# Kernel tuning notes

Measured on AMD Instinct MI355X. Metric: run time of the kernel, lower is better.

The kernel has to match this reference:

```python
import jax, jax.numpy as jnp
import numpy as np

EPS = 1e-06
NUM_HEADS = 16
HEAD_DIM = 72
HIDDEN = 1152
N = 4096


def _rms_norm(x, weight=None):
    # x: [..., head_dim]; computed in fp32 as in the torch reference
    xf = x.astype(jnp.float32)
    ms = jnp.mean(xf * xf, axis=-1, keepdims=True) + EPS
    y = xf * jax.lax.rsqrt(ms)
    if weight is not None:
        y = y * weight.astype(jnp.float32)
    return y.astype(x.dtype)


def _rotate_half(x):
    h = x.shape[-1] // 2
    return jnp.concatenate([-x[..., h:], x[..., :h]], axis=-1)


def _apply_2d_rope(x, cos, sin):
    # x: [n, H, head_dim]; cos/sin: [n, head_dim] (first half dim-0 freqs, second half dim-1)
    hd = x.shape[-1]
    x1, x2 = x[..., : hd // 2], x[..., hd // 2 :]
    c1, c2 = jnp.split(cos, 2, axis=-1)
    s1, s2 = jnp.split(sin, 2, axis=-1)

    def ap(xp, c, s):
        c = c[:, None, :]  # broadcast over heads (unsqueeze_dim=1)
        s = s[:, None, :]
        return xp * c + _rotate_half(xp) * s

    return jnp.concatenate([ap(x1, c1, s1), ap(x2, c2, s2)], axis=-1)


def setup_inputs() -> dict:
    key = jax.random.key(0)
    ks = jax.random.split(key, 8)
    hidden_states = jax.random.normal(ks[0], (N, HIDDEN), dtype=jnp.float32)
    cos = jax.random.uniform(ks[1], (N, HEAD_DIM), dtype=jnp.float32, minval=-1.0, maxval=1.0)
    sin = jax.random.uniform(ks[2], (N, HEAD_DIM), dtype=jnp.float32, minval=-1.0, maxval=1.0)
    proj = NUM_HEADS * HEAD_DIM
    Wq = jax.random.normal(ks[3], (HIDDEN, proj), dtype=jnp.float32) * 0.02
    Wk = jax.random.normal(ks[4], (HIDDEN, proj), dtype=jnp.float32) * 0.02
    Wv = jax.random.normal(ks[5], (HIDDEN, proj), dtype=jnp.float32) * 0.02
    Wo = jax.random.normal(ks[6], (proj, HIDDEN), dtype=jnp.float32) * 0.02
    q_scale = jnp.ones((HEAD_DIM,), dtype=jnp.float32)
    k_scale = jnp.ones((HEAD_DIM,), dtype=jnp.float32)
    return {
        "hidden_states": hidden_states, "cos": cos, "sin": sin,
        "Wq": Wq, "Wk": Wk, "Wv": Wv, "Wo": Wo,
        "q_scale": q_scale, "k_scale": k_scale,
    }


def reference(hidden_states, cos, sin, Wq, Wk, Wv, Wo, q_scale, k_scale):
    n = hidden_states.shape[0]
    xq = (hidden_states @ Wq).reshape(n, NUM_HEADS, HEAD_DIM)
    xk = (hidden_states @ Wk).reshape(n, NUM_HEADS, HEAD_DIM)
    xv = (hidden_states @ Wv).reshape(n, NUM_HEADS, HEAD_DIM)
    xq = _rms_norm(xq, q_scale)
    xk = _rms_norm(xk, k_scale)
    xv = _rms_norm(xv)  # no scale
    xq = _apply_2d_rope(xq, cos, sin)
    xk = _apply_2d_rope(xk, cos, sin)
    # eager bidirectional attention, scale = 1.0
    attn = jnp.einsum("nhd,mhd->hnm", xq, xk)  # [H, n, n]
    attn = jax.nn.softmax(attn.astype(jnp.float32), axis=-1).astype(xq.dtype)
    out = jnp.einsum("hnm,mhd->nhd", attn, xv)  # [n, H, d]
    out = out.reshape(n, NUM_HEADS * HEAD_DIM)
    return out @ Wo
```

## Files before the change

kernel.cpp:

```cpp
#include <hip/hip_runtime.h>
#include <stdint.h>

typedef unsigned short u16;
typedef __bf16 bf16x8 __attribute__((ext_vector_type(8)));
typedef float f32x4 __attribute__((ext_vector_type(4)));
typedef __attribute__((address_space(1))) const unsigned int as1_u32;
typedef __attribute__((address_space(3))) unsigned int as3_u32;

#define SEQ 4096
#define HID 1152
#define NH 16
#define HD 72

__device__ __forceinline__ void gload_lds16(const void* g, void* l) {
  __builtin_amdgcn_global_load_lds((as1_u32*)g, (as3_u32*)l, 16, 0, 0);
}
__device__ __forceinline__ u16 f2bf(float f) {
  __bf16 h = (__bf16)f;
  return __builtin_bit_cast(u16, h);
}
__device__ __forceinline__ float bf2f(u16 u) {
  unsigned int x = ((unsigned int)u) << 16;
  return __builtin_bit_cast(float, x);
}

__global__ void cvt_x(const float* __restrict__ X, u16* __restrict__ Xb, int n4) {
  int i = blockIdx.x * blockDim.x + threadIdx.x;
  if (i < n4) {
    float4 v = *(const float4*)(X + (size_t)i * 4);
    unsigned int lo = f2bf(v.x) | ((unsigned int)f2bf(v.y) << 16);
    unsigned int hi = f2bf(v.z) | ((unsigned int)f2bf(v.w) << 16);
    *(uint2*)(Xb + (size_t)i * 4) = make_uint2(lo, hi);
  }
}

__global__ void transpose_w(const float* __restrict__ Wq, const float* __restrict__ Wk,
                            const float* __restrict__ Wv, const float* __restrict__ Wo,
                            u16* __restrict__ Wt, u16* __restrict__ Wot) {
  __shared__ __align__(16) float t[32][33];
  int z = blockIdx.z;
  const float* src = (z == 0) ? Wq : (z == 1) ? Wk : (z == 2) ? Wv : Wo;
  u16* dst = (z < 3) ? (Wt + (size_t)z * HID * HID) : Wot;
  int tx = threadIdx.x & 31, ty = threadIdx.x >> 5;
  int c0 = blockIdx.x * 32, r0 = blockIdx.y * 32;
#pragma unroll
  for (int i = 0; i < 4; i++)
    t[ty + i * 8][tx] = src[(size_t)(r0 + ty + i * 8) * HID + c0 + tx];
  __syncthreads();
#pragma unroll
  for (int i = 0; i < 4; i++)
    dst[(size_t)(c0 + ty + i * 8) * HID + r0 + tx] = f2bf(t[tx][ty + i * 8]);
}

template <int OUTBF16>
__global__ __launch_bounds__(256, 2) void gemm_bt(const u16* __restrict__ A,
                                                  const u16* __restrict__ Bt,
                                                  void* __restrict__ Cout,
                                                  int M, int N, int K) {
  __shared__ __align__(16) u16 lds[2][2][128 * 64];
  const int tid = threadIdx.x;
  const int wave = tid >> 6, lane = tid & 63;
  const int l15 = lane & 15, l4 = lane >> 4;
  const size_t bm = (size_t)blockIdx.x * 128, bn = (size_t)blockIdx.y * 128;
  const int wm = (wave >> 1) * 64, wn = (wave & 1) * 64;
  const int nt = K >> 6;

  f32x4 acc[4][4] = {};

  auto stage = [&](int buf, int kt) {
    const int k0 = kt << 6;
#pragma unroll
    for (int r = 0; r < 4; r++) {
      int idx = (r << 8) + tid;
      int m = idx >> 3, j = idx & 7;
      int js = j ^ (m & 7);
      void* ldsA = (void*)&lds[buf][0][(size_t)((r << 8) + (wave << 6)) * 8];
      void* ldsB = (void*)&lds[buf][1][(size_t)((r << 8) + (wave << 6)) * 8];
      gload_lds16(A + (bm + m) * (size_t)K + k0 + js * 8, ldsA);
      gload_lds16(Bt + (bn + m) * (size_t)K + k0 + js * 8, ldsB);
    }
  };

  stage(0, 0);
  for (int t = 0; t < nt; t++) {
    __syncthreads();
    if (t + 1 < nt) stage((t + 1) & 1, t + 1);
    const u16* As = &lds[t & 1][0][0];
    const u16* Bs = &lds[t & 1][1][0];
#pragma unroll
    for (int kk = 0; kk < 2; kk++) {
      bf16x8 af[4], bfr[4];
      int slot = (kk << 2) + l4;
#pragma unroll
      for (int mi = 0; mi < 4; mi++) {
        int m = wm + (mi << 4) + l15;
        af[mi] = *(const bf16x8*)&As[m * 64 + ((slot ^ (m & 7)) << 3)];
      }
#pragma unroll
      for (int ni = 0; ni < 4; ni++) {
        int n = wn + (ni << 4) + l15;
        bfr[ni] = *(const bf16x8*)&Bs[n * 64 + ((slot ^ (n & 7)) << 3)];
      }
#pragma unroll
      for (int mi = 0; mi < 4; mi++)
#pragma unroll
        for (int ni = 0; ni < 4; ni++)
          acc[mi][ni] = __builtin_amdgcn_mfma_f32_16x16x32_bf16(af[mi], bfr[ni], acc[mi][ni], 0, 0, 0);
    }
  }

#pragma unroll
  for (int mi = 0; mi < 4; mi++)
#pragma unroll
    for (int ni = 0; ni < 4; ni++)
#pragma unroll
      for (int r = 0; r < 4; r++) {
        size_t m = bm + wm + (mi << 4) + (l4 << 2) + r;
        size_t n = bn + wn + (ni << 4) + l15;
        if (OUTBF16)
          ((u16*)Cout)[m * N + n] = f2bf(acc[mi][ni][r]);
        else
          ((float*)Cout)[m * N + n] = acc[mi][ni][r];
      }
}

__global__ __launch_bounds__(256, 2) void norm_rope(
    const u16* __restrict__ C1, const float* __restrict__ cosv,
    const float* __restrict__ sinv, const float* __restrict__ qsc,
    const float* __restrict__ ksc, u16* __restrict__ Qp, u16* __restrict__ Kp,
    u16* __restrict__ Vt) {
  __shared__ __align__(16) u16 in_t[32 * 224];
  __shared__ __align__(16) u16 qo[32 * 128];
  __shared__ __align__(16) u16 ko[32 * 128];
  __shared__ __align__(16) u16 vo[80 * 48];
  const int tid = threadIdx.x;
  const int h = blockIdx.y;
  const int n0 = blockIdx.x * 32;

#pragma unroll
  for (int k = 0; k < 4; k++) {
    int g = tid + k * 256;
    if (g < 864) {
      int row = g / 27, j = g - row * 27;
      int seg = j / 9, c = (j - seg * 9) * 8;
      const u16* src = C1 + (size_t)(n0 + row) * 3456 + seg * 1152 + h * HD + c;
      *(uint4*)&in_t[row * 224 + j * 8] = *(const uint4*)src;
    }
  }
  __syncthreads();

  const int r = tid >> 3, p = tid & 7;
  float sq = 0, sk = 0, sv = 0;
  auto acc8 = [&](int off, float& s) {
    uint4 v = *(const uint4*)&in_t[r * 224 + off];
    unsigned int vv[4] = {v.x, v.y, v.z, v.w};
#pragma unroll
    for (int q = 0; q < 4; q++) {
      float a = bf2f((u16)(vv[q] & 0xffff));
      float b = bf2f((u16)(vv[q] >> 16));
      s += a * a + b * b;
    }
  };
  acc8(0 + p * 8, sq);
  acc8(72 + p * 8, sk);
  acc8(144 + p * 8, sv);
  if (p == 0) { acc8(64, sq); acc8(136, sk); acc8(208, sv); }
#pragma unroll
  for (int m = 1; m < 8; m <<= 1) {
    sq += __shfl_xor(sq, m);
    sk += __shfl_xor(sk, m);
    sv += __shfl_xor(sv, m);
  }
  const float rq = rsqrtf(sq * (1.0f / 72.0f) + 1e-6f);
  const float rk = rsqrtf(sk * (1.0f / 72.0f) + 1e-6f);
  const float rv = rsqrtf(sv * (1.0f / 72.0f) + 1e-6f);

#pragma unroll
  for (int u = 0; u < 5; u++) {
    int ti = p + (u << 3);
    if (ti < 36) {
      int i1 = ti + ((ti >= 18) ? 18 : 0);
      int i2 = i1 + 18;
      const float* cb = cosv + (size_t)(n0 + r) * HD;
      const float* sb = sinv + (size_t)(n0 + r) * HD;
      float c1 = cb[i1], c2 = cb[i2], s1 = sb[i1], s2 = sb[i2];
      float q1 = bf2f(in_t[r * 224 + i1]) * rq * qsc[i1];
      float q2 = bf2f(in_t[r * 224 + i2]) * rq * qsc[i2];
      float k1 = bf2f(in_t[r * 224 + 72 + i1]) * rk * ksc[i1];
      float k2 = bf2f(in_t[r * 224 + 72 + i2]) * rk * ksc[i2];
      qo[r * 128 + i1] = f2bf(q1 * c1 - q2 * s1);
      qo[r * 128 + i2] = f2bf(q2 * c2 + q1 * s2);
      ko[r * 128 + i1] = f2bf(k1 * c1 - k2 * s1);
      ko[r * 128 + i2] = f2bf(k2 * c2 + k1 * s2);
    }
  }
#pragma unroll
  for (int u = 0; u < 9; u++) {
    int d = p * 9 + u;
    vo[d * 48 + r] = f2bf(bf2f(in_t[r * 224 + 144 + d]) * rv);
  }
  if (p < 7) {
    uint4 z = make_uint4(0, 0, 0, 0);
    *(uint4*)&qo[r * 128 + (9 + p) * 8] = z;
    *(uint4*)&ko[r * 128 + (9 + p) * 8] = z;
  }
  if (tid < 32) {
    int d = 72 + (tid >> 2), g = tid & 3;
    *(uint4*)&vo[d * 48 + g * 8] = make_uint4(0, 0, 0, 0);
  }
  __syncthreads();

#pragma unroll
  for (int k = 0; k < 2; k++) {
    int g = tid + k * 256;
    int row = g >> 4, j = g & 15;
    *(uint4*)(Qp + ((size_t)h * SEQ + n0 + row) * 128 + j * 8) = *(const uint4*)&qo[row * 128 + j * 8];
    *(uint4*)(Kp + ((size_t)h * SEQ + n0 + row) * 128 + j * 8) = *(const uint4*)&ko[row * 128 + j * 8];
  }
#pragma unroll
  for (int k = 0; k < 2; k++) {
    int g = tid + k * 256;
    if (g < 320) {
      int d = g >> 2, j = g & 3;
      *(uint4*)(Vt + ((size_t)h * 80 + d) * SEQ + n0 + j * 8) = *(const uint4*)&vo[d * 48 + j * 8];
    }
  }
}

__global__ __launch_bounds__(256, 2) void attn(const u16* __restrict__ Qp,
                                               const u16* __restrict__ Kp,
                                               const u16* __restrict__ Vt,
                                               u16* __restrict__ AO) {
  __shared__ __align__(16) u16 Ks[2][64 * 128];
  __shared__ __align__(16) u16 Vs[2][80 * 64];
  __shared__ __align__(16) u16 Ps[4][32 * 64];
  const int tid = threadIdx.x;
  const int wave = tid >> 6, lane = tid & 63;
  const int l15 = lane & 15, l4 = lane >> 4;
  const int h = blockIdx.y;
  const int q0 = blockIdx.x * 128 + wave * 32;

  bf16x8 bq[2][3];
#pragma unroll
  for (int qf = 0; qf < 2; qf++) {
    const u16* qbase = Qp + ((size_t)h * SEQ + q0 + qf * 16 + l15) * 128;
#pragma unroll
    for (int kk = 0; kk < 3; kk++) bq[qf][kk] = *(const bf16x8*)(qbase + kk * 32 + l4 * 8);
  }

  f32x4 acc[2][5] = {};
  float mi_[2] = {-1e30f, -1e30f};
  float li_[2] = {0.0f, 0.0f};

  auto stage = [&](int buf, int k0) {
#pragma unroll
    for (int rr = 0; rr < 4; rr++) {
      int g = (rr << 8) + tid;
      int m = g >> 4, j = g & 15;
      int js = j ^ (m & 15);
      gload_lds16(Kp + ((size_t)h * SEQ + k0 + m) * 128 + js * 8,
                  (void*)&Ks[buf][(size_t)((rr << 8) + (wave << 6)) * 8]);
    }
#pragma unroll
    for (int rr = 0; rr < 3; rr++) {
      int c = (rr << 2) + wave;
      if (c < 10) {
        int g = (c << 6) + lane;
        int d = g >> 3, j = g & 7;
        int js = j ^ (d & 7);
        gload_lds16(Vt + ((size_t)h * 80 + d) * SEQ + k0 + js * 8,
                    (void*)&Vs[buf][(size_t)(c << 6) * 8]);
      }
    }
  };

  stage(0, 0);
  for (int t = 0; t < 64; t++) {
    __syncthreads();
    if (t < 63) stage((t + 1) & 1, (t + 1) * 64);
    const u16* Kb = Ks[t & 1];
    const u16* Vb = Vs[t & 1];

    f32x4 s[2][4] = {};
#pragma unroll
    for (int kk = 0; kk < 3; kk++) {
      int slot = (kk << 2) + l4;
      bf16x8 ak[4];
#pragma unroll
      for (int nf = 0; nf < 4; nf++) {
        int row = (nf << 4) + l15;
        ak[nf] = *(const bf16x8*)&Kb[row * 128 + ((slot ^ (row & 15)) << 3)];
      }
#pragma unroll
      for (int qf = 0; qf < 2; qf++)
#pragma unroll
        for (int nf = 0; nf < 4; nf++)
          s[qf][nf] = __builtin_amdgcn_mfma_f32_16x16x32_bf16(ak[nf], bq[qf][kk], s[qf][nf], 0, 0, 0);
    }

    float scl[2];
#pragma unroll
    for (int qf = 0; qf < 2; qf++) {
      float v0 = fmaxf(fmaxf(s[qf][0][0], s[qf][0][1]), fmaxf(s[qf][0][2], s[qf][0][3]));
      float v1 = fmaxf(fmaxf(s[qf][1][0], s[qf][1][1]), fmaxf(s[qf][1][2], s[qf][1][3]));
      float v2 = fmaxf(fmaxf(s[qf][2][0], s[qf][2][1]), fmaxf(s[qf][2][2], s[qf][2][3]));
      float v3 = fmaxf(fmaxf(s[qf][3][0], s[qf][3][1]), fmaxf(s[qf][3][2], s[qf][3][3]));
      float v = fmaxf(fmaxf(v0, v1), fmaxf(v2, v3));
      v = fmaxf(v, __shfl_xor(v, 16));
      v = fmaxf(v, __shfl_xor(v, 32));
      float mnew = fmaxf(mi_[qf], v);
      scl[qf] = __expf(mi_[qf] - mnew);
      mi_[qf] = mnew;
      float rsum = 0.0f;
      int row = (qf << 4) + l15;
#pragma unroll
      for (int nf = 0; nf < 4; nf++) {
        ushort4 pk;
        float p0 = __expf(s[qf][nf][0] - mnew);
        float p1 = __expf(s[qf][nf][1] - mnew);
        float p2 = __expf(s[qf][nf][2] - mnew);
        float p3 = __expf(s[qf][nf][3] - mnew);
        rsum += (p0 + p1) + (p2 + p3);
        pk.x = f2bf(p0); pk.y = f2bf(p1); pk.z = f2bf(p2); pk.w = f2bf(p3);
        int gg = (nf << 2) + l4;
        int gs = gg ^ ((row & 7) << 1);
        *(ushort4*)&Ps[wave][row * 64 + gs * 4] = pk;
      }
      rsum += __shfl_xor(rsum, 16);
      rsum += __shfl_xor(rsum, 32);
      li_[qf] = li_[qf] * scl[qf] + rsum;
    }

#pragma unroll
    for (int qf = 0; qf < 2; qf++)
#pragma unroll
      for (int r = 0; r < 4; r++) {
        float sr = __shfl(scl[qf], (l4 << 2) + r);
#pragma unroll
        for (int ni = 0; ni < 5; ni++) acc[qf][ni][r] *= sr;
      }

#pragma unroll
    for (int kk = 0; kk < 2; kk++) {
      bf16x8 pa[2];
#pragma unroll
      for (int qf = 0; qf < 2; qf++) {
        int row = (qf << 4) + l15;
        int gb = ((kk << 3) + (l4 << 1)) ^ ((row & 7) << 1);
        pa[qf] = *(const bf16x8*)&Ps[wave][row * 64 + gb * 4];
      }
      int slot = (kk << 2) + l4;
#pragma unroll
      for (int ni = 0; ni < 5; ni++) {
        int d = (ni << 4) + l15;
        bf16x8 bv = *(const bf16x8*)&Vb[d * 64 + ((slot ^ (d & 7)) << 3)];
#pragma unroll
        for (int qf = 0; qf < 2; qf++)
          acc[qf][ni] = __builtin_amdgcn_mfma_f32_16x16x32_bf16(pa[qf], bv, acc[qf][ni], 0, 0, 0);
      }
    }
  }

#pragma unroll
  for (int qf = 0; qf < 2; qf++)
#pragma unroll
    for (int r = 0; r < 4; r++) {
      float inv = 1.0f / __shfl(li_[qf], (l4 << 2) + r);
      int q = q0 + (qf << 4) + (l4 << 2) + r;
#pragma unroll
      for (int ni = 0; ni < 5; ni++) {
        int d = (ni << 4) + l15;
        if (d < HD) AO[(size_t)q * HID + h * HD + d] = f2bf(acc[qf][ni][r] * inv);
      }
    }
}

extern "C" void kernel_launch(void* const* d_in, const int* in_sizes, int n_in,
                              void* d_out, int out_size, void* d_ws, size_t ws_size,
                              hipStream_t stream) {
  const float* X = (const float*)d_in[0];
  const float* cosv = (const float*)d_in[1];
  const float* sinv = (const float*)d_in[2];
  const float* Wq = (const float*)d_in[3];
  const float* Wk = (const float*)d_in[4];
  const float* Wv = (const float*)d_in[5];
  const float* Wo = (const float*)d_in[6];
  const float* qsc = (const float*)d_in[7];
  const float* ksc = (const float*)d_in[8];
  float* out = (float*)d_out;

  uint8_t* ws = (uint8_t*)d_ws;
  u16* Xb  = (u16*)(ws);
  u16* Wt  = (u16*)(ws + 9437184);
  u16* Wot = (u16*)(ws + 17399808);
  u16* C1  = (u16*)(ws + 20054016);
  u16* Qp  = (u16*)(ws + 48365568);
  u16* Kp  = (u16*)(ws + 65142784);
  u16* Vt  = (u16*)(ws + 81920000);
  u16* AO  = Xb;

  cvt_x<<<4608, 256, 0, stream>>>(X, Xb, (SEQ * HID) / 4);
  transpose_w<<<dim3(36, 36, 4), 256, 0, stream>>>(Wq, Wk, Wv, Wo, Wt, Wot);
  gemm_bt<1><<<dim3(32, 27), 256, 0, stream>>>(Xb, Wt, (void*)C1, SEQ, 3456, HID);
  norm_rope<<<dim3(128, 16), 256, 0, stream>>>(C1, cosv, sinv, qsc, ksc, Qp, Kp, Vt);
  attn<<<dim3(32, 16), 256, 0, stream>>>(Qp, Kp, Vt, AO);
  gemm_bt<0><<<dim3(32, 9), 256, 0, stream>>>(AO, Wot, (void*)out, SEQ, HID, HID);
}
```

Before: 343.8 us.

## Tune attention: lazy rescale, deferred row-sum reduce, head remap, setprio, narrower Q

Several attention-loop changes land together. The online-softmax rescale of the accumulator is skipped when no row maximum grew, and the row-sum cross-lane reduction moves out of the loop to the epilogue. Scheduling priority is raised around the MFMA blocks, and blocks are remapped so neighbouring blocks handle different heads. Q is stored with a 96-element row stride, V staging is restructured and the workspace offsets shift; this adds a divergent branch and more complexity to the loop.

```diff
diff --git a/kernel.cpp b/kernel.cpp
--- a/kernel.cpp
+++ b/kernel.cpp
@@ -130,8 +130,8 @@
     const float* __restrict__ ksc, u16* __restrict__ Qp, u16* __restrict__ Kp,
     u16* __restrict__ Vt) {
   __shared__ __align__(16) u16 in_t[32 * 224];
-  __shared__ __align__(16) u16 qo[32 * 128];
-  __shared__ __align__(16) u16 ko[32 * 128];
+  __shared__ __align__(16) u16 qo[32 * 96];
+  __shared__ __align__(16) u16 ko[32 * 96];
   __shared__ __align__(16) u16 vo[80 * 48];
   const int tid = threadIdx.x;
   const int h = blockIdx.y;
@@ -188,10 +188,10 @@
       float q2 = bf2f(in_t[r * 224 + i2]) * rq * qsc[i2];
       float k1 = bf2f(in_t[r * 224 + 72 + i1]) * rk * ksc[i1];
       float k2 = bf2f(in_t[r * 224 + 72 + i2]) * rk * ksc[i2];
-      qo[r * 128 + i1] = f2bf(q1 * c1 - q2 * s1);
-      qo[r * 128 + i2] = f2bf(q2 * c2 + q1 * s2);
-      ko[r * 128 + i1] = f2bf(k1 * c1 - k2 * s1);
-      ko[r * 128 + i2] = f2bf(k2 * c2 + k1 * s2);
+      qo[r * 96 + i1] = f2bf(q1 * c1 - q2 * s1);
+      qo[r * 96 + i2] = f2bf(q2 * c2 + q1 * s2);
+      ko[r * 96 + i1] = f2bf(k1 * c1 - k2 * s1);
+      ko[r * 96 + i2] = f2bf(k2 * c2 + k1 * s2);
     }
   }
 #pragma unroll
@@ -199,10 +199,10 @@
     int d = p * 9 + u;
     vo[d * 48 + r] = f2bf(bf2f(in_t[r * 224 + 144 + d]) * rv);
   }
-  if (p < 7) {
+  if (p < 3) {
     uint4 z = make_uint4(0, 0, 0, 0);
-    *(uint4*)&qo[r * 128 + (9 + p) * 8] = z;
-    *(uint4*)&ko[r * 128 + (9 + p) * 8] = z;
+    *(uint4*)&qo[r * 96 + (9 + p) * 8] = z;
+    *(uint4*)&ko[r * 96 + (9 + p) * 8] = z;
   }
   if (tid < 32) {
     int d = 72 + (tid >> 2), g = tid & 3;
@@ -213,9 +213,11 @@
 #pragma unroll
   for (int k = 0; k < 2; k++) {
     int g = tid + k * 256;
-    int row = g >> 4, j = g & 15;
-    *(uint4*)(Qp + ((size_t)h * SEQ + n0 + row) * 128 + j * 8) = *(const uint4*)&qo[row * 128 + j * 8];
-    *(uint4*)(Kp + ((size_t)h * SEQ + n0 + row) * 128 + j * 8) = *(const uint4*)&ko[row * 128 + j * 8];
+    if (g < 384) {
+      int row = g / 12, j = g - row * 12;
+      *(uint4*)(Qp + ((size_t)h * SEQ + n0 + row) * 96 + j * 8) = *(const uint4*)&qo[row * 96 + j * 8];
+      *(uint4*)(Kp + ((size_t)h * SEQ + n0 + row) * 128 + j * 8) = *(const uint4*)&ko[row * 96 + j * 8];
+    }
   }
 #pragma unroll
   for (int k = 0; k < 2; k++) {
@@ -237,13 +239,16 @@
   const int tid = threadIdx.x;
   const int wave = tid >> 6, lane = tid & 63;
   const int l15 = lane & 15, l4 = lane >> 4;
-  const int h = blockIdx.y;
-  const int q0 = blockIdx.x * 128 + wave * 32;
+
+  const int bid = blockIdx.x + (blockIdx.y << 5);
+  const int h = ((bid & 7) << 1) | ((bid >> 3) & 1);
+  const int qt = bid >> 4;
+  const int q0 = qt * 128 + wave * 32;
 
   bf16x8 bq[2][3];
 #pragma unroll
   for (int qf = 0; qf < 2; qf++) {
-    const u16* qbase = Qp + ((size_t)h * SEQ + q0 + qf * 16 + l15) * 128;
+    const u16* qbase = Qp + ((size_t)h * SEQ + q0 + (qf << 4) + l15) * 96;
 #pragma unroll
     for (int kk = 0; kk < 3; kk++) bq[qf][kk] = *(const bf16x8*)(qbase + kk * 32 + l4 * 8);
   }
@@ -254,23 +259,27 @@
 
   auto stage = [&](int buf, int k0) {
 #pragma unroll
-    for (int rr = 0; rr < 4; rr++) {
-      int g = (rr << 8) + tid;
+    for (int i = 0; i < 4; i++) {
+      int g = tid + (i << 8);
       int m = g >> 4, j = g & 15;
       int js = j ^ (m & 15);
       gload_lds16(Kp + ((size_t)h * SEQ + k0 + m) * 128 + js * 8,
-                  (void*)&Ks[buf][(size_t)((rr << 8) + (wave << 6)) * 8]);
-    }
-#pragma unroll
-    for (int rr = 0; rr < 3; rr++) {
-      int c = (rr << 2) + wave;
-      if (c < 10) {
-        int g = (c << 6) + lane;
-        int d = g >> 3, j = g & 7;
-        int js = j ^ (d & 7);
-        gload_lds16(Vt + ((size_t)h * 80 + d) * SEQ + k0 + js * 8,
-                    (void*)&Vs[buf][(size_t)(c << 6) * 8]);
-      }
+                  (void*)&Ks[buf][(size_t)((i << 8) + (wave << 6)) * 8]);
+    }
+#pragma unroll
+    for (int i = 0; i < 2; i++) {
+      int g = tid + (i << 8);
+      int d = g >> 3, j = g & 7;
+      int js = j ^ (d & 7);
+      gload_lds16(Vt + ((size_t)h * 80 + d) * SEQ + k0 + js * 8,
+                  (void*)&Vs[buf][(size_t)((i << 8) + (wave << 6)) * 8]);
+    }
+    if (wave < 2) {
+      int g = tid + 512;
+      int d = g >> 3, j = g & 7;
+      int js = j ^ (d & 7);
+      gload_lds16(Vt + ((size_t)h * 80 + d) * SEQ + k0 + js * 8,
+                  (void*)&Vs[buf][(size_t)(512 + (wave << 6)) * 8]);
     }
   };
 
@@ -282,6 +291,7 @@
     const u16* Vb = Vs[t & 1];
 
     f32x4 s[2][4] = {};
+    __builtin_amdgcn_s_setprio(1);
 #pragma unroll
     for (int kk = 0; kk < 3; kk++) {
       int slot = (kk << 2) + l4;
@@ -289,16 +299,16 @@
 #pragma unroll
       for (int nf = 0; nf < 4; nf++) {
         int row = (nf << 4) + l15;
-        ak[nf] = *(const bf16x8*)&Kb[row * 128 + ((slot ^ (row & 15)) << 3)];
-      }
-#pragma unroll
-      for (int qf = 0; qf < 2; qf++)
-#pragma unroll
-        for (int nf = 0; nf < 4; nf++)
-          s[qf][nf] = __builtin_amdgcn_mfma_f32_16x16x32_bf16(ak[nf], bq[qf][kk], s[qf][nf], 0, 0, 0);
-    }
-
-    float scl[2];
+        ak[nf] = *(const bf16x8*)&Kb[row * 128 + ((slot ^ l15) << 3)];
+      }
+#pragma unroll
+      for (int nf = 0; nf < 4; nf++) {
+        s[0][nf] = __builtin_amdgcn_mfma_f32_16x16x32_bf16(ak[nf], bq[0][kk], s[0][nf], 0, 0, 0);
+        s[1][nf] = __builtin_amdgcn_mfma_f32_16x16x32_bf16(ak[nf], bq[1][kk], s[1][nf], 0, 0, 0);
+      }
+    }
+    __builtin_amdgcn_s_setprio(0);
+
 #pragma unroll
     for (int qf = 0; qf < 2; qf++) {
       float v0 = fmaxf(fmaxf(s[qf][0][0], s[qf][0][1]), fmaxf(s[qf][0][2], s[qf][0][3]));
@@ -308,9 +318,19 @@
       float v = fmaxf(fmaxf(v0, v1), fmaxf(v2, v3));
       v = fmaxf(v, __shfl_xor(v, 16));
       v = fmaxf(v, __shfl_xor(v, 32));
-      float mnew = fmaxf(mi_[qf], v);
-      scl[qf] = __expf(mi_[qf] - mnew);
-      mi_[qf] = mnew;
+      if (!__all(v <= mi_[qf])) {
+        float mnew = fmaxf(mi_[qf], v);
+        float scl = __expf(mi_[qf] - mnew);
+        mi_[qf] = mnew;
+        li_[qf] *= scl;
+#pragma unroll
+        for (int r = 0; r < 4; r++) {
+          float sr = __shfl(scl, (l4 << 2) + r);
+#pragma unroll
+          for (int ni = 0; ni < 5; ni++) acc[qf][ni][r] *= sr;
+        }
+      }
+      float mnew = mi_[qf];
       float rsum = 0.0f;
       int row = (qf << 4) + l15;
 #pragma unroll
@@ -322,24 +342,13 @@
         float p3 = __expf(s[qf][nf][3] - mnew);
         rsum += (p0 + p1) + (p2 + p3);
         pk.x = f2bf(p0); pk.y = f2bf(p1); pk.z = f2bf(p2); pk.w = f2bf(p3);
-        int gg = (nf << 2) + l4;
-        int gs = gg ^ ((row & 7) << 1);
+        int gs = ((nf << 2) + l4) ^ ((row & 7) << 1);
         *(ushort4*)&Ps[wave][row * 64 + gs * 4] = pk;
       }
-      rsum += __shfl_xor(rsum, 16);
-      rsum += __shfl_xor(rsum, 32);
-      li_[qf] = li_[qf] * scl[qf] + rsum;
-    }
-
-#pragma unroll
-    for (int qf = 0; qf < 2; qf++)
-#pragma unroll
-      for (int r = 0; r < 4; r++) {
-        float sr = __shfl(scl[qf], (l4 << 2) + r);
-#pragma unroll
-        for (int ni = 0; ni < 5; ni++) acc[qf][ni][r] *= sr;
-      }
-
+      li_[qf] += rsum;
+    }
+
+    __builtin_amdgcn_s_setprio(1);
 #pragma unroll
     for (int kk = 0; kk < 2; kk++) {
       bf16x8 pa[2];
@@ -354,18 +363,21 @@
       for (int ni = 0; ni < 5; ni++) {
         int d = (ni << 4) + l15;
         bf16x8 bv = *(const bf16x8*)&Vb[d * 64 + ((slot ^ (d & 7)) << 3)];
-#pragma unroll
-        for (int qf = 0; qf < 2; qf++)
-          acc[qf][ni] = __builtin_amdgcn_mfma_f32_16x16x32_bf16(pa[qf], bv, acc[qf][ni], 0, 0, 0);
-      }
-    }
-  }
-
-#pragma unroll
-  for (int qf = 0; qf < 2; qf++)
+        acc[0][ni] = __builtin_amdgcn_mfma_f32_16x16x32_bf16(pa[0], bv, acc[0][ni], 0, 0, 0);
+        acc[1][ni] = __builtin_amdgcn_mfma_f32_16x16x32_bf16(pa[1], bv, acc[1][ni], 0, 0, 0);
+      }
+    }
+    __builtin_amdgcn_s_setprio(0);
+  }
+
+#pragma unroll
+  for (int qf = 0; qf < 2; qf++) {
+    float li = li_[qf];
+    li += __shfl_xor(li, 16);
+    li += __shfl_xor(li, 32);
 #pragma unroll
     for (int r = 0; r < 4; r++) {
-      float inv = 1.0f / __shfl(li_[qf], (l4 << 2) + r);
+      float inv = 1.0f / __shfl(li, (l4 << 2) + r);
       int q = q0 + (qf << 4) + (l4 << 2) + r;
 #pragma unroll
       for (int ni = 0; ni < 5; ni++) {
@@ -373,6 +385,7 @@
         if (d < HD) AO[(size_t)q * HID + h * HD + d] = f2bf(acc[qf][ni][r] * inv);
       }
     }
+  }
 }
 
 extern "C" void kernel_launch(void* const* d_in, const int* in_sizes, int n_in,
@@ -395,8 +408,8 @@
   u16* Wot = (u16*)(ws + 17399808);
   u16* C1  = (u16*)(ws + 20054016);
   u16* Qp  = (u16*)(ws + 48365568);
-  u16* Kp  = (u16*)(ws + 65142784);
-  u16* Vt  = (u16*)(ws + 81920000);
+  u16* Kp  = (u16*)(ws + 60948480);
+  u16* Vt  = (u16*)(ws + 77725696);
   u16* AO  = Xb;
 
   cvt_x<<<4608, 256, 0, stream>>>(X, Xb, (SEQ * HID) / 4);
```

Measured after the change: 321.7 us. -6.4%, faster.
